# Performance work log

Measured on AMD Instinct MI355X. Metric: run time of the kernel, lower is better.

## Reference

```python
import jax, jax.numpy as jnp
import numpy as np

HEADS = 16

def setup_inputs() -> dict:
    key = jax.random.key(0)
    k1, k2, k3 = jax.random.split(key, 3)
    B, E, W = 4, 1024, 2048
    x = jax.random.normal(k1, (B, E, W), dtype=jnp.float32)
    # dense Linear params (bias=True): M ~ randn * ((E+E)/2)^-0.5, b ~ randn / E^2
    M_d = jax.random.normal(k2, (E, E), dtype=jnp.float32) * (E ** -0.5)
    b_d = jax.random.normal(k3, (E,), dtype=jnp.float32) / (E ** 2)
    return {"x": x, "M_d": M_d, "b_d": b_d}


def reference(x, M_d, b_d):
    B, E, W = x.shape
    H = HEADS
    D = E // H
    # NOTE: original code computes self.linear(x) but discards it (KQV = x.view)
    kqv = x.reshape(B, H, D, W)  # [B,H,D,W]
    # scores[b,h,i,j] = sum_d kqv[b,h,d,i]*kqv[b,h,d,j], scaled by E^-0.5
    scores = jnp.einsum('bhdi,bhdj->bhij', kqv, kqv) * (E ** -0.5)
    # causal_factor = tril(ones, diagonal=-1): mask strictly-lower (i>j) to -inf
    i = jnp.arange(W)[:, None]
    j = jnp.arange(W)[None, :]
    scores = jnp.where(i > j, -jnp.inf, scores)
    # softmax over axis -2 (over i, per column j)
    att = jax.nn.softmax(scores, axis=-2)  # [B,H,W,W]
    t = jnp.einsum('bhdi,bhij->bhdj', kqv, att)  # [B,H,D,W]
    t = t.reshape(B, E, W)
    # dense Linear: (B,W,E) @ M + b, transposed back to (B,E,W)
    out = jnp.einsum('bew,ef->bfw', t, M_d) + b_d[None, :, None]
    return out
```

## Files before the change

### kernel.cpp

```cpp
#include <hip/hip_runtime.h>
#include <hip/hip_bf16.h>

constexpr int B  = 4;
constexpr int E  = 1024;
constexpr int Wn = 2048;
constexpr int H  = 16;
constexpr int Dh = 64;

typedef short bf16x8 __attribute__((ext_vector_type(8)));
typedef float f32x4  __attribute__((ext_vector_type(4)));

__device__ inline unsigned short f2bf(float f){
    unsigned int u = __builtin_bit_cast(unsigned int, f);
    u = (u + 0x7fffu + ((u >> 16) & 1u)) >> 16;
    return (unsigned short)u;
}
__device__ inline float bf2f(unsigned short u){
    return __builtin_bit_cast(float, (unsigned int)u << 16);
}
__device__ inline unsigned int pack_bf16_trunc(float lo, float hi){
    return __builtin_amdgcn_perm(__builtin_bit_cast(unsigned int, hi),
                                 __builtin_bit_cast(unsigned int, lo), 0x07060302u);
}
__device__ inline float exp2_fast(float x){ return __builtin_amdgcn_exp2f(x); }
__device__ inline int SW(int c){ return c ^ (((c >> 5) & 7) << 2); }

#define GLDS(g, l) __builtin_amdgcn_global_load_lds( \
    (const __attribute__((address_space(1))) void*)(g), \
    (__attribute__((address_space(3))) void*)(l), 16, 0, 0)

__device__ __constant__ signed char SB2T[19] =
    {2,1,3,3,5,5,5,7,7,7,7,4,4,6,6,6,6,4,0};
__device__ __constant__ signed char KV64T[19] =
    {0,0,0,8,0,8,16,0,8,16,24,0,7,0,7,14,21,14,0};
__device__ __constant__ signed char NSTT[19] =
    {12,8,8,8,8,8,8,8,8,8,8,7,7,7,7,7,7,6,4};
__device__ __constant__ signed char SLOTT[19] =
    {-1,-1,0,1,5,6,7,12,13,14,15,2,3,8,9,10,11,4,-1};
__device__ __constant__ signed char LASTT[19] =
    {1,1,0,1,0,0,1,0,0,0,1,0,0,0,0,0,1,1,1};
__device__ __constant__ signed char NCHT[5]   = {2,3,3,4,4};
__device__ __constant__ signed char SBASET[5] = {0,2,5,8,12};

__global__ __launch_bounds__(256) void k_prep(const float* __restrict__ x,
                                              unsigned short* __restrict__ xS,
                                              unsigned short* __restrict__ xdi){
    __shared__ float tile[64*257];
    const float cs = 0.2123304349f;
    const int t  = threadIdx.x;
    const int bh = blockIdx.x >> 3;
    const int w0 = (blockIdx.x & 7) << 8;

    {
        const int r = t >> 2, seg = t & 3;
        const float* src = x + ((size_t)bh*64 + r)*Wn + w0 + seg*64;
        float* dst = tile + r*257;
        #pragma unroll
        for (int i = 0; i < 16; ++i){
            float4 v = *reinterpret_cast<const float4*>(src + i*4);
            int c0 = seg*64 + i*4;
            dst[SW(c0+0)] = v.x; dst[SW(c0+1)] = v.y;
            dst[SW(c0+2)] = v.z; dst[SW(c0+3)] = v.w;
        }
    }
    __syncthreads();

    {
        const int kgw = t & 3, g = (t >> 2) & 7, r0 = t >> 5;
        #pragma unroll
        for (int rr = 0; rr < 8; ++rr){
            const int r = r0*8 + rr;
            const float* base = tile + r*257;
            const int c0 = g*32 + 4*kgw;
            union { unsigned short us[8]; uint4 v; } u;
            #pragma unroll
            for (int j2 = 0; j2 < 4; ++j2){
                u.us[j2]   = f2bf(base[SW(c0 + j2)]);
                u.us[4+j2] = f2bf(base[SW(c0 + 16 + j2)]);
            }
            *reinterpret_cast<uint4*>(xdi + ((size_t)bh*64 + r)*Wn + w0 + g*32 + 8*kgw) = u.v;
        }
    }
    {
        const int w = t;
        #pragma unroll
        for (int dg = 0; dg < 8; ++dg){
            union { unsigned short us[8]; uint4 v; } u;
            #pragma unroll
            for (int i = 0; i < 8; ++i)
                u.us[i] = f2bf(tile[(dg*8 + i)*257 + SW(w)] * cs);
            *reinterpret_cast<uint4*>(xS + ((size_t)bh*Wn + w0 + w)*64 + dg*8) = u.v;
        }
    }
}

__global__ void k_MT(const float* __restrict__ M, unsigned short* __restrict__ MT){
    int tid = blockIdx.x*256 + threadIdx.x;
    int f  = tid & (E-1);
    int eg = tid >> 10;
    union { unsigned short us[8]; uint4 v; } u;
    #pragma unroll
    for (int i = 0; i < 8; i++) u.us[i] = f2bf(M[(size_t)(eg*8+i)*E + f]);
    *reinterpret_cast<uint4*>(MT + (size_t)f*E + eg*8) = u.v;
}

__global__ __launch_bounds__(512)
void k_attn(const unsigned short* __restrict__ xS,
            const unsigned short* __restrict__ xdi,
            unsigned short* __restrict__ tws,
            unsigned short* __restrict__ pacc,
            float* __restrict__ pl){
    __shared__ char Klds[3*8192];
    __shared__ char Vlds[3*8192];

    const int lane = threadIdx.x & 63;
    const int wv   = threadIdx.x >> 6;
    const int jl = lane & 15, kg = lane >> 4;
    const int sw = jl & 7;

    const int p    = blockIdx.x;
    const int xcd  = p & 7;
    const int hh   = (p >> 3) & 7;
    const int widx = p >> 6;
    const int bh   = xcd*8 + hh;

    const int sb2  = SB2T[widx];
    const int kvb  = (int)KV64T[widx] * 64;
    const int nst  = NSTT[widx];
    const int slot = SLOTT[widx];
    const bool isLast = LASTT[widx] != 0;

    const int q0w = sb2*256 + wv*32;

    const bf16x8* xSr = reinterpret_cast<const bf16x8*>(xS + (size_t)bh*Wn*Dh);
    bf16x8 bq[2][2];
    #pragma unroll
    for (int jt = 0; jt < 2; jt++){
        bq[jt][0] = xSr[(q0w + jt*16 + jl)*8 + kg];
        bq[jt][1] = xSr[(q0w + jt*16 + jl)*8 + 4 + kg];
    }
    union { bf16x8 v; unsigned short us[8]; } ones;
    #pragma unroll
    for (int i2 = 0; i2 < 8; i2++) ones.us[i2] = 0x3F80;

    f32x4 acc[2][4] = {};
    f32x4 accl[2] = {};

    const char* Kg = (const char*)xS  + (size_t)bh*Wn*128;
    const char* Vg = (const char*)xdi + (size_t)bh*Dh*(Wn*2);
    const int rloc = 8*wv + (lane >> 3);
    const int ksw  = ((lane & 7) ^ (rloc & 7))*16;

    auto STAGE = [&](int buf, int kvT){
        const char* kg0 = Kg + (size_t)(kvT + rloc)*128 + ksw;
        const char* vg0 = Vg + (size_t)rloc*(Wn*2) + kvT*2 + ksw;
        GLDS(kg0, Klds + buf*8192 + wv*1024);
        GLDS(vg0, Vlds + buf*8192 + wv*1024);
    };

    auto computeS = [&](int buf, int s, bool dg){
        const char* Kb = Klds + buf*8192;
        const char* Vb = Vlds + buf*8192;
        const int r0 = s*32 + jl, r1 = r0 + 16;
        bf16x8 k0a = *(const bf16x8*)(Kb + r0*128 + ((kg    )^sw)*16);
        bf16x8 k0b = *(const bf16x8*)(Kb + r0*128 + ((kg + 4)^sw)*16);
        bf16x8 k1a = *(const bf16x8*)(Kb + r1*128 + ((kg    )^sw)*16);
        bf16x8 k1b = *(const bf16x8*)(Kb + r1*128 + ((kg + 4)^sw)*16);
        const int vsw = ((s*4 + kg)^sw)*16;
        bf16x8 v0 = *(const bf16x8*)(Vb + (     jl)*128 + vsw);
        bf16x8 v1 = *(const bf16x8*)(Vb + (16 + jl)*128 + vsw);
        bf16x8 v2 = *(const bf16x8*)(Vb + (32 + jl)*128 + vsw);
        bf16x8 v3 = *(const bf16x8*)(Vb + (48 + jl)*128 + vsw);

        #pragma unroll
        for (int jt = 0; jt < 2; jt++){
            f32x4 s0 = {0,0,0,0}, s1 = {0,0,0,0};
            s0 = __builtin_amdgcn_mfma_f32_16x16x32_bf16(k0a, bq[jt][0], s0, 0,0,0);
            s0 = __builtin_amdgcn_mfma_f32_16x16x32_bf16(k0b, bq[jt][1], s0, 0,0,0);
            s1 = __builtin_amdgcn_mfma_f32_16x16x32_bf16(k1a, bq[jt][0], s1, 0,0,0);
            s1 = __builtin_amdgcn_mfma_f32_16x16x32_bf16(k1b, bq[jt][1], s1, 0,0,0);

            union { bf16x8 v; unsigned int w[4]; } bp;
            if (!dg){
                bp.w[0] = pack_bf16_trunc(exp2_fast(s0[0]), exp2_fast(s0[1]));
                bp.w[1] = pack_bf16_trunc(exp2_fast(s0[2]), exp2_fast(s0[3]));
                bp.w[2] = pack_bf16_trunc(exp2_fast(s1[0]), exp2_fast(s1[1]));
                bp.w[3] = pack_bf16_trunc(exp2_fast(s1[2]), exp2_fast(s1[3]));
            } else {
                const int lim = 16*jt + jl;
                float pp[8];
                #pragma unroll
                for (int r = 0; r < 4; r++){
                    int c = 4*kg + r;
                    pp[r]   = (c      <= lim) ? exp2_fast(s0[r]) : 0.f;
                    pp[4+r] = (c + 16 <= lim) ? exp2_fast(s1[r]) : 0.f;
                }
                bp.w[0] = pack_bf16_trunc(pp[0], pp[1]);
                bp.w[1] = pack_bf16_trunc(pp[2], pp[3]);
                bp.w[2] = pack_bf16_trunc(pp[4], pp[5]);
                bp.w[3] = pack_bf16_trunc(pp[6], pp[7]);
            }
            accl[jt] = __builtin_amdgcn_mfma_f32_16x16x32_bf16(ones.v, bp.v, accl[jt], 0,0,0);
            acc[jt][0] = __builtin_amdgcn_mfma_f32_16x16x32_bf16(v0, bp.v, acc[jt][0], 0,0,0);
            acc[jt][1] = __builtin_amdgcn_mfma_f32_16x16x32_bf16(v1, bp.v, acc[jt][1], 0,0,0);
            acc[jt][2] = __builtin_amdgcn_mfma_f32_16x16x32_bf16(v2, bp.v, acc[jt][2], 0,0,0);
            acc[jt][3] = __builtin_amdgcn_mfma_f32_16x16x32_bf16(v3, bp.v, acc[jt][3], 0,0,0);
        }
    };

    STAGE(0, kvb);
    if (nst > 1) STAGE(1, kvb + 64);
    int cur = 0;
    for (int t = 0; t < nst; ++t){
        const int kvT = kvb + 64*t;
        if (t + 1 < nst){
            asm volatile("s_waitcnt vmcnt(2)" ::: "memory");
        } else {
            asm volatile("s_waitcnt vmcnt(0)" ::: "memory");
        }
        __builtin_amdgcn_s_barrier();
        __builtin_amdgcn_sched_barrier(0);
        if (t + 2 < nst){
            const int nb = (cur >= 1) ? cur - 1 : cur + 2;
            STAGE(nb, kvT + 128);
        }
        __builtin_amdgcn_s_setprio(1);
        #pragma unroll
        for (int s = 0; s < 2; ++s){
            const int kv = kvT + 32*s;
            if (kv > q0w) continue;
            computeS(cur, s, isLast && (kv == q0w));
        }
        __builtin_amdgcn_s_setprio(0);
        cur = (cur == 2) ? 0 : cur + 1;
    }

    if (slot < 0){
        #pragma unroll
        for (int jt = 0; jt < 2; jt++){
            const float inv = 1.0f / accl[jt][0];
            unsigned short* trow = tws + ((size_t)(bh >> 4)*Wn + q0w + jt*16 + jl)*E + (bh & 15)*Dh;
            #pragma unroll
            for (int dt = 0; dt < 4; dt++){
                union { unsigned short us[4]; ushort4 v; } o;
                #pragma unroll
                for (int r = 0; r < 4; r++) o.us[r] = f2bf(acc[jt][dt][r] * inv);
                *reinterpret_cast<ushort4*>(trow + dt*16 + 4*kg) = o.v;
            }
        }
    } else {
        const int gslot = bh*16 + slot;
        if (kg == 0){
            pl[(size_t)gslot*256 + wv*32 + jl]      = accl[0][0];
            pl[(size_t)gslot*256 + wv*32 + 16 + jl] = accl[1][0];
        }
        unsigned short* pa = pacc + (size_t)gslot*16384;
        #pragma unroll
        for (int jt = 0; jt < 2; jt++){
            #pragma unroll
            for (int dt = 0; dt < 4; dt++){
                union { unsigned short us[4]; ushort4 v; } o;
                #pragma unroll
                for (int r = 0; r < 4; r++) o.us[r] = f2bf(acc[jt][dt][r]);
                *reinterpret_cast<ushort4*>(pa + (wv*32 + jt*16 + jl)*64 + dt*16 + 4*kg) = o.v;
            }
        }
    }
}

__global__ __launch_bounds__(512) void k_reduce(const unsigned short* __restrict__ pacc,
                                                const float* __restrict__ pl,
                                                unsigned short* __restrict__ tws){
    const int g   = blockIdx.x;
    const int bh  = g / 5, s5 = g % 5;
    const int sb2 = 3 + s5;
    const int t   = threadIdx.x;
    const int qq  = t >> 1;
    const int db  = (t & 1)*32;
    const int nch   = NCHT[s5];
    const int slot0 = bh*16 + SBASET[s5];

    float l = 0.f;
    float a[32];
    #pragma unroll
    for (int i = 0; i < 32; ++i) a[i] = 0.f;
    for (int c = 0; c < nch; ++c){
        l += pl[(size_t)(slot0 + c)*256 + qq];
        const unsigned short* pa = pacc + (size_t)(slot0 + c)*16384 + qq*64 + db;
        #pragma unroll
        for (int i = 0; i < 4; ++i){
            union { uint4 v; unsigned short us[8]; } r0;
            r0.v = *reinterpret_cast<const uint4*>(pa + i*8);
            #pragma unroll
            for (int j2 = 0; j2 < 8; ++j2) a[i*8 + j2] += bf2f(r0.us[j2]);
        }
    }
    const float inv = 1.0f / l;
    unsigned short* tw = tws + ((size_t)(bh >> 4)*Wn + sb2*256 + qq)*E + (bh & 15)*Dh + db;
    #pragma unroll
    for (int i = 0; i < 4; ++i){
        union { uint4 v; unsigned short us[8]; } o;
        #pragma unroll
        for (int j2 = 0; j2 < 8; ++j2) o.us[j2] = f2bf(a[i*8 + j2] * inv);
        *reinterpret_cast<uint4*>(tw + i*8) = o.v;
    }
}

__global__ __launch_bounds__(256)
void k_gemm(const unsigned short* __restrict__ MT,
            const unsigned short* __restrict__ tws,
            const float* __restrict__ bd,
            float* __restrict__ out){
    __shared__ char Alds[2*16384];
    __shared__ char Blds[2*16384];

    const int lane = threadIdx.x & 63;
    const int wv   = threadIdx.x >> 6;
    const int jl = lane & 15, kg = lane >> 4;
    const int sw = jl & 7;

    const int p   = blockIdx.x;
    const int blk = (p & 7)*64 + (p >> 3);
    const int b  = blk >> 7;
    const int t2 = blk & 127;
    const int fblk = (t2 >> 4)*128;
    const int wblk = (t2 & 15)*128;
    const int f0 = fblk + (wv >> 1)*64;
    const int w0 = wblk + (wv &  1)*64;

    const char* Ag = (const char*)MT + (size_t)fblk*E*2;
    const char* Bg = (const char*)tws + ((size_t)b*Wn + wblk)*E*2;
    const int rloc = 8*wv + (lane >> 3);
    const int scw  = ((lane & 7) ^ (lane >> 3))*16;

    auto STAGE = [&](int buf, int e0){
        char* Ab = Alds + buf*16384;
        char* Bb = Blds + buf*16384;
        const char* ag = Ag + (size_t)rloc*(E*2) + e0*2 + scw;
        const char* bg = Bg + (size_t)rloc*(E*2) + e0*2 + scw;
        #pragma unroll
        for (int g = 0; g < 4; ++g){
            GLDS(ag + (size_t)g*32*(E*2), Ab + g*4096 + wv*1024);
            GLDS(bg + (size_t)g*32*(E*2), Bb + g*4096 + wv*1024);
        }
    };

    f32x4 acc[4][4] = {};

    auto COMP = [&](int buf){
        const char* Ab = Alds + buf*16384 + ((wv >> 1)*64)*128;
        const char* Bb = Blds + buf*16384 + ((wv &  1)*64)*128;
        #pragma unroll
        for (int h = 0; h < 2; ++h){
            const int cs = ((h*4 + kg) ^ sw)*16;
            bf16x8 am[4], bn[4];
            #pragma unroll
            for (int i = 0; i < 4; i++) am[i] = *(const bf16x8*)(Ab + (i*16 + jl)*128 + cs);
            #pragma unroll
            for (int j = 0; j < 4; j++) bn[j] = *(const bf16x8*)(Bb + (j*16 + jl)*128 + cs);
            #pragma unroll
            for (int i = 0; i < 4; i++)
                #pragma unroll
                for (int j = 0; j < 4; j++)
                    acc[i][j] = __builtin_amdgcn_mfma_f32_16x16x32_bf16(am[i], bn[j], acc[i][j], 0,0,0);
        }
    };

    STAGE(0, 0);
    for (int t = 0; t < 16; ++t){
        if (t < 15){
            STAGE((t+1)&1, (t+1)*64);
            asm volatile("s_waitcnt vmcnt(8)" ::: "memory");
        } else {
            asm volatile("s_waitcnt vmcnt(0)" ::: "memory");
        }
        __builtin_amdgcn_s_barrier();
        __builtin_amdgcn_sched_barrier(0);
        __builtin_amdgcn_s_setprio(1);
        COMP(t & 1);
        __builtin_amdgcn_s_setprio(0);
        asm volatile("s_waitcnt lgkmcnt(0)" ::: "memory");
        __builtin_amdgcn_sched_barrier(0);
        __builtin_amdgcn_s_barrier();
    }

    #pragma unroll
    for (int i = 0; i < 4; i++){
        float bias[4];
        #pragma unroll
        for (int r = 0; r < 4; r++) bias[r] = bd[f0 + i*16 + 4*kg + r];
        #pragma unroll
        for (int j = 0; j < 4; j++){
            #pragma unroll
            for (int r = 0; r < 4; r++){
                out[((size_t)b*E + f0 + i*16 + 4*kg + r)*Wn + w0 + j*16 + jl]
                    = acc[i][j][r] + bias[r];
            }
        }
    }
}

extern "C" void kernel_launch(void* const* d_in, const int* in_sizes, int n_in,
                              void* d_out, int out_size, void* d_ws, size_t ws_size,
                              hipStream_t stream) {
    const float* x  = (const float*)d_in[0];
    const float* Md = (const float*)d_in[1];
    const float* bd = (const float*)d_in[2];
    float* out = (float*)d_out;

    char* ws = (char*)d_ws;
    unsigned short* xS   = (unsigned short*)(ws);
    unsigned short* xdi  = (unsigned short*)(ws + (16u << 20));
    unsigned short* MT   = (unsigned short*)(ws + (32u << 20));
    unsigned short* tws  = (unsigned short*)(ws + (34u << 20));
    float*          pl   = (float*)(ws + (50u << 20));
    unsigned short* pacc = (unsigned short*)d_out;

    hipLaunchKernelGGL(k_prep,   dim3(512),  dim3(256), 0, stream, x, xS, xdi);
    hipLaunchKernelGGL(k_MT,     dim3(512),  dim3(256), 0, stream, Md, MT);
    hipLaunchKernelGGL(k_attn,   dim3(19*64), dim3(512), 0, stream, xS, xdi, tws, pacc, pl);
    hipLaunchKernelGGL(k_reduce, dim3(320),  dim3(512), 0, stream, pacc, pl, tws);
    hipLaunchKernelGGL(k_gemm,   dim3(B*(E/128)*(Wn/128)), dim3(256), 0, stream, MT, tws, bd, out);
}
```

Baseline: 107.5 us.

## Give each attention wave 64 query columns and rebalance split-KV work table

The attention kernel now launches 256-thread blocks of four waves, and each wave owns 64 query columns instead of 32. Every K/V tile loaded into LDS is therefore reused by twice as many query rows per wave, and each wave issues two async LDS loads per tile. The static split-KV schedule is rebuilt with 15 work items per head instead of 19, more evenly sized at 12, 8 or 4 stages, which changes the partial slot count and the reduce indexing. The cost is double the accumulator registers per wave, which may lower occupancy, plus a new causal-mask path driven by a query offset.

After: 138.3 us. 1.29x slower.

```diff
diff --git a/kernel.cpp b/kernel.cpp
--- a/kernel.cpp
+++ b/kernel.cpp
@@ -29,18 +29,13 @@
     (const __attribute__((address_space(1))) void*)(g), \
     (__attribute__((address_space(3))) void*)(l), 16, 0, 0)
 
-__device__ __constant__ signed char SB2T[19] =
-    {2,1,3,3,5,5,5,7,7,7,7,4,4,6,6,6,6,4,0};
-__device__ __constant__ signed char KV64T[19] =
-    {0,0,0,8,0,8,16,0,8,16,24,0,7,0,7,14,21,14,0};
-__device__ __constant__ signed char NSTT[19] =
-    {12,8,8,8,8,8,8,8,8,8,8,7,7,7,7,7,7,6,4};
-__device__ __constant__ signed char SLOTT[19] =
-    {-1,-1,0,1,5,6,7,12,13,14,15,2,3,8,9,10,11,4,-1};
-__device__ __constant__ signed char LASTT[19] =
-    {1,1,0,1,0,0,1,0,0,0,1,0,0,0,0,0,1,1,1};
-__device__ __constant__ signed char NCHT[5]   = {2,3,3,4,4};
-__device__ __constant__ signed char SBASET[5] = {0,2,5,8,12};
+__device__ __constant__ signed char SB2T[15]  = {2,4,5,5,6,7,7, 1,3,3,4,6,6,7, 0};
+__device__ __constant__ signed char KV64T[15] = {0,0,0,12,0,0,12, 0,0,8,12,12,20,24, 0};
+__device__ __constant__ signed char NSTT[15]  = {12,12,12,12,12,12,12, 8,8,8,8,8,8,8, 4};
+__device__ __constant__ signed char SLOTT[15] = {-1,2,4,5,6,9,10, -1,0,1,3,7,8,11, -1};
+__device__ __constant__ signed char LASTT[15] = {1,0,0,1,0,0,0, 1,0,1,1,0,1,1, 1};
+__device__ __constant__ signed char NCHT[5]   = {2,2,2,3,3};
+__device__ __constant__ signed char SBASET[5] = {0,2,4,6,9};
 
 __global__ __launch_bounds__(256) void k_prep(const float* __restrict__ x,
                                               unsigned short* __restrict__ xS,
@@ -104,7 +99,7 @@
     *reinterpret_cast<uint4*>(MT + (size_t)f*E + eg*8) = u.v;
 }
 
-__global__ __launch_bounds__(512)
+__global__ __launch_bounds__(256)
 void k_attn(const unsigned short* __restrict__ xS,
             const unsigned short* __restrict__ xdi,
             unsigned short* __restrict__ tws,
@@ -130,12 +125,12 @@
     const int slot = SLOTT[widx];
     const bool isLast = LASTT[widx] != 0;
 
-    const int q0w = sb2*256 + wv*32;
+    const int q0w = sb2*256 + wv*64;
 
     const bf16x8* xSr = reinterpret_cast<const bf16x8*>(xS + (size_t)bh*Wn*Dh);
-    bf16x8 bq[2][2];
-    #pragma unroll
-    for (int jt = 0; jt < 2; jt++){
+    bf16x8 bq[4][2];
+    #pragma unroll
+    for (int jt = 0; jt < 4; jt++){
         bq[jt][0] = xSr[(q0w + jt*16 + jl)*8 + kg];
         bq[jt][1] = xSr[(q0w + jt*16 + jl)*8 + 4 + kg];
     }
@@ -143,22 +138,24 @@
     #pragma unroll
     for (int i2 = 0; i2 < 8; i2++) ones.us[i2] = 0x3F80;
 
-    f32x4 acc[2][4] = {};
-    f32x4 accl[2] = {};
+    f32x4 acc[4][4] = {};
+    f32x4 accl[4] = {};
 
     const char* Kg = (const char*)xS  + (size_t)bh*Wn*128;
     const char* Vg = (const char*)xdi + (size_t)bh*Dh*(Wn*2);
-    const int rloc = 8*wv + (lane >> 3);
-    const int ksw  = ((lane & 7) ^ (rloc & 7))*16;
+    const int rloc = 16*wv + (lane >> 3);
+    const int ksw  = ((lane & 7) ^ (lane >> 3))*16;
 
     auto STAGE = [&](int buf, int kvT){
         const char* kg0 = Kg + (size_t)(kvT + rloc)*128 + ksw;
         const char* vg0 = Vg + (size_t)rloc*(Wn*2) + kvT*2 + ksw;
-        GLDS(kg0, Klds + buf*8192 + wv*1024);
-        GLDS(vg0, Vlds + buf*8192 + wv*1024);
+        GLDS(kg0,                    Klds + buf*8192 + wv*2048);
+        GLDS(kg0 + 8*128,            Klds + buf*8192 + wv*2048 + 1024);
+        GLDS(vg0,                    Vlds + buf*8192 + wv*2048);
+        GLDS(vg0 + (size_t)8*(Wn*2), Vlds + buf*8192 + wv*2048 + 1024);
     };
 
-    auto computeS = [&](int buf, int s, bool dg){
+    auto computeS = [&](int buf, int s, int offq){
         const char* Kb = Klds + buf*8192;
         const char* Vb = Vlds + buf*8192;
         const int r0 = s*32 + jl, r1 = r0 + 16;
@@ -173,7 +170,7 @@
         bf16x8 v3 = *(const bf16x8*)(Vb + (48 + jl)*128 + vsw);
 
         #pragma unroll
-        for (int jt = 0; jt < 2; jt++){
+        for (int jt = 0; jt < 4; jt++){
             f32x4 s0 = {0,0,0,0}, s1 = {0,0,0,0};
             s0 = __builtin_amdgcn_mfma_f32_16x16x32_bf16(k0a, bq[jt][0], s0, 0,0,0);
             s0 = __builtin_amdgcn_mfma_f32_16x16x32_bf16(k0b, bq[jt][1], s0, 0,0,0);
@@ -181,13 +178,13 @@
             s1 = __builtin_amdgcn_mfma_f32_16x16x32_bf16(k1b, bq[jt][1], s1, 0,0,0);
 
             union { bf16x8 v; unsigned int w[4]; } bp;
-            if (!dg){
+            if (offq >= 32){
                 bp.w[0] = pack_bf16_trunc(exp2_fast(s0[0]), exp2_fast(s0[1]));
                 bp.w[1] = pack_bf16_trunc(exp2_fast(s0[2]), exp2_fast(s0[3]));
                 bp.w[2] = pack_bf16_trunc(exp2_fast(s1[0]), exp2_fast(s1[1]));
                 bp.w[3] = pack_bf16_trunc(exp2_fast(s1[2]), exp2_fast(s1[3]));
             } else {
-                const int lim = 16*jt + jl;
+                const int lim = offq + 16*jt + jl;
                 float pp[8];
                 #pragma unroll
                 for (int r = 0; r < 4; r++){
@@ -200,7 +197,7 @@
                 bp.w[2] = pack_bf16_trunc(pp[4], pp[5]);
                 bp.w[3] = pack_bf16_trunc(pp[6], pp[7]);
             }
-            accl[jt] = __builtin_amdgcn_mfma_f32_16x16x32_bf16(ones.v, bp.v, accl[jt], 0,0,0);
+            accl[jt]   = __builtin_amdgcn_mfma_f32_16x16x32_bf16(ones.v, bp.v, accl[jt], 0,0,0);
             acc[jt][0] = __builtin_amdgcn_mfma_f32_16x16x32_bf16(v0, bp.v, acc[jt][0], 0,0,0);
             acc[jt][1] = __builtin_amdgcn_mfma_f32_16x16x32_bf16(v1, bp.v, acc[jt][1], 0,0,0);
             acc[jt][2] = __builtin_amdgcn_mfma_f32_16x16x32_bf16(v2, bp.v, acc[jt][2], 0,0,0);
@@ -209,12 +206,12 @@
     };
 
     STAGE(0, kvb);
-    if (nst > 1) STAGE(1, kvb + 64);
+    STAGE(1, kvb + 64);
     int cur = 0;
     for (int t = 0; t < nst; ++t){
         const int kvT = kvb + 64*t;
         if (t + 1 < nst){
-            asm volatile("s_waitcnt vmcnt(2)" ::: "memory");
+            asm volatile("s_waitcnt vmcnt(4)" ::: "memory");
         } else {
             asm volatile("s_waitcnt vmcnt(0)" ::: "memory");
         }
@@ -225,11 +222,17 @@
             STAGE(nb, kvT + 128);
         }
         __builtin_amdgcn_s_setprio(1);
-        #pragma unroll
-        for (int s = 0; s < 2; ++s){
-            const int kv = kvT + 32*s;
-            if (kv > q0w) continue;
-            computeS(cur, s, isLast && (kv == q0w));
+        if (!isLast){
+            computeS(cur, 0, 64);
+            computeS(cur, 1, 64);
+        } else {
+            #pragma unroll
+            for (int s = 0; s < 2; ++s){
+                const int kv = kvT + 32*s;
+                const int offq = q0w - kv;
+                if (offq <= -64) continue;
+                computeS(cur, s, offq);
+            }
         }
         __builtin_amdgcn_s_setprio(0);
         cur = (cur == 2) ? 0 : cur + 1;
@@ -237,7 +240,7 @@
 
     if (slot < 0){
         #pragma unroll
-        for (int jt = 0; jt < 2; jt++){
+        for (int jt = 0; jt < 4; jt++){
             const float inv = 1.0f / accl[jt][0];
             unsigned short* trow = tws + ((size_t)(bh >> 4)*Wn + q0w + jt*16 + jl)*E + (bh & 15)*Dh;
             #pragma unroll
@@ -249,20 +252,21 @@
             }
         }
     } else {
-        const int gslot = bh*16 + slot;
+        const int gslot = bh*12 + slot;
         if (kg == 0){
-            pl[(size_t)gslot*256 + wv*32 + jl]      = accl[0][0];
-            pl[(size_t)gslot*256 + wv*32 + 16 + jl] = accl[1][0];
+            #pragma unroll
+            for (int jt = 0; jt < 4; jt++)
+                pl[(size_t)gslot*256 + wv*64 + jt*16 + jl] = accl[jt][0];
         }
         unsigned short* pa = pacc + (size_t)gslot*16384;
         #pragma unroll
-        for (int jt = 0; jt < 2; jt++){
+        for (int jt = 0; jt < 4; jt++){
             #pragma unroll
             for (int dt = 0; dt < 4; dt++){
                 union { unsigned short us[4]; ushort4 v; } o;
                 #pragma unroll
                 for (int r = 0; r < 4; r++) o.us[r] = f2bf(acc[jt][dt][r]);
-                *reinterpret_cast<ushort4*>(pa + (wv*32 + jt*16 + jl)*64 + dt*16 + 4*kg) = o.v;
+                *reinterpret_cast<ushort4*>(pa + (wv*64 + jt*16 + jl)*64 + dt*16 + 4*kg) = o.v;
             }
         }
     }
@@ -278,7 +282,7 @@
     const int qq  = t >> 1;
     const int db  = (t & 1)*32;
     const int nch   = NCHT[s5];
-    const int slot0 = bh*16 + SBASET[s5];
+    const int slot0 = bh*12 + SBASET[s5];
 
     float l = 0.f;
     float a[32];
@@ -418,7 +422,7 @@
 
     hipLaunchKernelGGL(k_prep,   dim3(512),  dim3(256), 0, stream, x, xS, xdi);
     hipLaunchKernelGGL(k_MT,     dim3(512),  dim3(256), 0, stream, Md, MT);
-    hipLaunchKernelGGL(k_attn,   dim3(19*64), dim3(512), 0, stream, xS, xdi, tws, pacc, pl);
+    hipLaunchKernelGGL(k_attn,   dim3(15*64), dim3(256), 0, stream, xS, xdi, tws, pacc, pl);
     hipLaunchKernelGGL(k_reduce, dim3(320),  dim3(512), 0, stream, pacc, pl, tws);
     hipLaunchKernelGGL(k_gemm,   dim3(B*(E/128)*(Wn/128)), dim3(256), 0, stream, MT, tws, bd, out);
 }
```
